# Kernel optimization log

Hardware: AMD Instinct MI355X
Metric: run time of the kernel (lower is better)

## Reference

```python
import jax, jax.numpy as jnp
import numpy as np

S, B, D, H, WIN, L = 8192, 4, 512, 8, 64, 6
HD = D // H
EPS = 1e-5


def setup_inputs() -> dict:
    key = jax.random.key(0)
    ks = jax.random.split(key, 6)
    s = 0.02
    return {
        "src": jax.random.normal(ks[0], (S, B, D), jnp.float32),
        "Wqkv": jax.random.normal(ks[1], (L, 3 * D, D), jnp.float32) * s,
        "bqkv": jnp.zeros((L, 3 * D), jnp.float32),
        "Wo": jax.random.normal(ks[2], (L, D, D), jnp.float32) * s,
        "bo": jnp.zeros((L, D), jnp.float32),
        "W1": jax.random.normal(ks[3], (L, 4 * D, D), jnp.float32) * s,
        "bf1": jnp.zeros((L, 4 * D), jnp.float32),
        "W2": jax.random.normal(ks[4], (L, D, 4 * D), jnp.float32) * s,
        "bf2": jnp.zeros((L, D), jnp.float32),
        "g1": jnp.ones((L, D), jnp.float32),
        "beta1": jnp.zeros((L, D), jnp.float32),
        "g2": jnp.ones((L, D), jnp.float32),
        "beta2": jnp.zeros((L, D), jnp.float32),
    }


def layernorm(x, g, b):
    m = jnp.mean(x, axis=-1, keepdims=True)
    v = jnp.mean(jnp.square(x - m), axis=-1, keepdims=True)
    return (x - m) * jax.lax.rsqrt(v + EPS) * g + b


def _forward(src, Wqkv, bqkv, Wo, bo, W1, bf1, W2, bf2, g1, beta1, g2, beta2):
    NW = S // WIN
    scale = 1.0 / np.sqrt(HD)
    x = src
    for l in range(L):
        qkv = x @ Wqkv[l].T + bqkv[l]                      # (S,B,3D)
        q, k, v = jnp.split(qkv, 3, axis=-1)
        win = lambda t: t.reshape(NW, WIN, B, H, HD)       # (NW,W,B,H,hd)
        q = win(q) * scale
        k = win(k)
        v = win(v)
        att = jax.nn.softmax(jnp.einsum('nqbhd,nkbhd->nbhqk', q, k), axis=-1)
        o = jnp.einsum('nbhqk,nkbhd->nqbhd', att, v).reshape(S, B, D)
        o = o @ Wo[l].T + bo[l]
        x = layernorm(x + o, g1[l], beta1[l])
        # FFN with ReLU (hidden = 4*d_model)
        f = jax.nn.relu(x @ W1[l].T + bf1[l]) @ W2[l].T + bf2[l]
        x = layernorm(x + f, g2[l], beta2[l])
    return x


def reference(src, Wqkv, bqkv, Wo, bo, W1, bf1, W2, bf2, g1, beta1, g2, beta2):
    return _forward(src, Wqkv, bqkv, Wo, bo, W1, bf1, W2, bf2, g1, beta1, g2, beta2)
```

## Files before the change

### kernel.cpp

```cpp
#include <hip/hip_runtime.h>
#include <hip/hip_bf16.h>

typedef __bf16 bf16x8 __attribute__((ext_vector_type(8)));
typedef float f32x4 __attribute__((ext_vector_type(4)));

static constexpr int NT = 32768;
static constexpr int D_ = 512;
static constexpr int D3 = 1536;
static constexpr int DF = 2048;
static constexpr int L_ = 6;

#define AS1 __attribute__((address_space(1)))
#define AS3 __attribute__((address_space(3)))

__device__ __forceinline__ void gload_lds16(const void* g, void* l) {
  __builtin_amdgcn_global_load_lds((const AS1 void*)g, (AS3 void*)l, 16, 0, 0);
}

template<int K, int NTN, bool RELU>
__global__ __launch_bounds__(256, 3) void gemm128g(
    const __hip_bfloat16* __restrict__ A,
    const __hip_bfloat16* __restrict__ Wp,
    const float* __restrict__ bias,
    __hip_bfloat16* __restrict__ Cout) {
  __shared__ __align__(16) char lds[32768];
  const int t = threadIdx.x;
  const int l = t & 63, w = t >> 6;
  const int lrow = l & 15, lhi = l >> 4;
  const int wr = w >> 1, wc = w & 1;

  const int lin = blockIdx.x;
  const int wg = (lin & 7) * ((int)gridDim.x >> 3) + (lin >> 3);
  const int tm0 = (wg / NTN) * 128, tn0 = (wg % NTN) * 128;

  constexpr int NKT = K / 64;
  constexpr int NIT = NKT / 2;
  constexpr int N = NTN * 128;

  const int srow = t >> 3;
  const int sun = t & 7;
  const int u8 = (sun ^ (srow & 7)) << 3;
  const __hip_bfloat16* sA = A + (size_t)(tm0 + srow) * K + u8;
  const __hip_bfloat16* sA2 = sA + (size_t)64 * K;

  const char* bpB = (const char*)(Wp + (size_t)((tn0 >> 6) + wc) * NKT * 4096) +
                    l * 16;

  const int lo = lrow * 128;
  const int x0 = (lhi ^ (lrow & 7)) << 4;
  const int x1 = ((4 + lhi) ^ (lrow & 7)) << 4;
  const char* pA[2][2];
  pA[0][0] = lds + wr * 8192 + lo + x0;
  pA[0][1] = lds + wr * 8192 + lo + x1;
  pA[1][0] = lds + 16384 + wr * 8192 + lo + x0;
  pA[1][1] = lds + 16384 + wr * 8192 + lo + x1;

  auto stageA = [&](int p, const __hip_bfloat16* s0, const __hip_bfloat16* s1) {
    char* d0 = lds + p * 16384 + w * 1024;
    gload_lds16(s0, d0);
    gload_lds16(s0 + (size_t)32 * K, d0 + 4096);
    char* d1 = lds + p * 16384 + 8192 + w * 1024;
    gload_lds16(s1, d1);
    gload_lds16(s1 + (size_t)32 * K, d1 + 4096);
  };
  auto loadB = [&](bf16x8 (&bf)[4][2], const char* q) {
    const char* q2 = q + 4096;
#pragma unroll
    for (int n = 0; n < 2; ++n)
#pragma unroll
      for (int ks = 0; ks < 2; ++ks) {
        bf[n][ks] = *(const bf16x8*)(q + (n * 2 + ks) * 1024);
        bf[2 + n][ks] = *(const bf16x8*)(q2 + (n * 2 + ks) * 1024);
      }
  };

  f32x4 acc[4][4] = {};
  bf16x8 bfA[4][2], bfB[4][2], af[2][2];

  stageA(0, sA, sA2);
  __builtin_amdgcn_sched_barrier(0);
  loadB(bfA, bpB);
  asm volatile("s_waitcnt vmcnt(8)" ::: "memory");
  __builtin_amdgcn_sched_barrier(0);
  __builtin_amdgcn_s_barrier();

#define SUB(P, BF, MB)                                                      \
  {                                                                          \
    _Pragma("unroll") for (int ks = 0; ks < 2; ++ks) {                       \
      af[0][ks] = *(const bf16x8*)(pA[P][ks] + (MB) * 2048);                 \
      af[1][ks] = *(const bf16x8*)(pA[P][ks] + (MB + 1) * 2048);             \
    }                                                                        \
    _Pragma("unroll") for (int n = 0; n < 4; ++n)                            \
        _Pragma("unroll") for (int ks = 0; ks < 2; ++ks) {                   \
      acc[MB][n] = __builtin_amdgcn_mfma_f32_16x16x32_bf16(                  \
          af[0][ks], BF[n][ks], acc[MB][n], 0, 0, 0);                        \
      acc[MB + 1][n] = __builtin_amdgcn_mfma_f32_16x16x32_bf16(              \
          af[1][ks], BF[n][ks], acc[MB + 1][n], 0, 0, 0);                    \
    }                                                                        \
  }
#define CLOSE(VM)                                                           \
  if (VM) asm volatile("s_waitcnt vmcnt(8)" ::: "memory");                  \
  else asm volatile("s_waitcnt vmcnt(0)" ::: "memory");                     \
  asm volatile("s_waitcnt lgkmcnt(0)" ::: "memory");                        \
  __builtin_amdgcn_sched_barrier(0);                                        \
  __builtin_amdgcn_s_barrier();

  const __hip_bfloat16* sAe = sA;
  const __hip_bfloat16* sA2e = sA2;
  const char* qbe = bpB;
  for (int it = 0; it < NIT; ++it) {
    const bool more = (it + 1 < NIT);
    stageA(1, sAe + 64, sA2e + 64);
    __builtin_amdgcn_sched_barrier(0);
    loadB(bfB, qbe + 8192);
    SUB(0, bfA, 0)
    SUB(0, bfA, 2)
    CLOSE(1)
    if (more) {
      stageA(0, sAe + 128, sA2e + 128);
      __builtin_amdgcn_sched_barrier(0);
      loadB(bfA, qbe + 16384);
    }
    SUB(1, bfB, 0)
    SUB(1, bfB, 2)
    CLOSE(more)
    sAe += 128;
    sA2e += 128;
    qbe += 16384;
  }
#undef SUB
#undef CLOSE

  char* ep = lds + w * 8192;
#pragma unroll
  for (int n = 0; n < 4; ++n) {
    float bv = bias[tn0 + wc * 64 + n * 16 + lrow];
#pragma unroll
    for (int m = 0; m < 4; ++m)
#pragma unroll
      for (int j = 0; j < 4; ++j) {
        float v = acc[m][n][j] + bv;
        if (RELU) v = fmaxf(v, 0.f);
        int row = m * 16 + lhi * 4 + j;
        int col = n * 16 + lrow;
        *(__hip_bfloat16*)(ep + row * 128 + (((col >> 3) ^ (row & 7)) << 4) +
                           (col & 7) * 2) = __float2bfloat16(v);
      }
  }
  __builtin_amdgcn_sched_barrier(0);
  const int er = l >> 3, ec = l & 7;
#pragma unroll
  for (int q = 0; q < 8; ++q) {
    int r = q * 8 + er;
    uint4 vv = *(const uint4*)(ep + r * 128 + ((ec ^ (r & 7)) << 4));
    *(uint4*)&Cout[(size_t)(tm0 + wr * 64 + r) * N + tn0 + wc * 64 + ec * 8] = vv;
  }
}

__global__ __launch_bounds__(128) void attn_win(
    const __hip_bfloat16* __restrict__ qkv, __hip_bfloat16* __restrict__ o) {
  __shared__ __align__(16) char lds[2 * 18432];
  const int t = threadIdx.x, l = t & 63, w = t >> 6;
  char* vt = lds + w * 18432;
  char* pl = vt + 9216;
  const int wid = blockIdx.x * 2 + w;
  const int h = wid & 7, b = (wid >> 3) & 3, nw = wid >> 5;
  const int lrow = l & 15, lhi = l >> 4;
  const __hip_bfloat16* qp = qkv + (size_t)(nw * 256 + b) * 1536 + h * 64;
  const __hip_bfloat16* kp = qp + 512;
  const __hip_bfloat16* vp = qp + 1024;

  {
    const int d0 = (l & 7) * 8;
    const int r0 = l >> 3;
#pragma unroll
    for (int i = 0; i < 8; ++i) {
      int r = r0 + i * 8;
      union { uint4 u; __hip_bfloat16 e[8]; } vv;
      vv.u = *(const uint4*)(vp + (size_t)r * 6144 + d0);
#pragma unroll
      for (int j = 0; j < 8; ++j)
        *(__hip_bfloat16*)(vt + ((d0 + j) * 72 + r) * 2) = vv.e[j];
    }
  }

  bf16x8 qf[4][2], kf[4][2];
#pragma unroll
  for (int mi = 0; mi < 4; ++mi)
#pragma unroll
    for (int ks = 0; ks < 2; ++ks) {
      int r = mi * 16 + lrow;
      int d = ks * 32 + lhi * 8;
      qf[mi][ks] = __builtin_bit_cast(bf16x8, *(const uint4*)(qp + (size_t)r * 6144 + d));
      kf[mi][ks] = __builtin_bit_cast(bf16x8, *(const uint4*)(kp + (size_t)r * 6144 + d));
    }

  f32x4 s[4][4] = {};
#pragma unroll
  for (int mi = 0; mi < 4; ++mi)
#pragma unroll
    for (int ni = 0; ni < 4; ++ni) {
      s[mi][ni] = __builtin_amdgcn_mfma_f32_16x16x32_bf16(qf[mi][0], kf[ni][0], s[mi][ni], 0, 0, 0);
      s[mi][ni] = __builtin_amdgcn_mfma_f32_16x16x32_bf16(qf[mi][1], kf[ni][1], s[mi][ni], 0, 0, 0);
    }

#pragma unroll
  for (int mi = 0; mi < 4; ++mi)
#pragma unroll
    for (int j = 0; j < 4; ++j) {
      float mx = s[mi][0][j];
#pragma unroll
      for (int ni = 1; ni < 4; ++ni) mx = fmaxf(mx, s[mi][ni][j]);
      mx = fmaxf(mx, __shfl_xor(mx, 1));
      mx = fmaxf(mx, __shfl_xor(mx, 2));
      mx = fmaxf(mx, __shfl_xor(mx, 4));
      mx = fmaxf(mx, __shfl_xor(mx, 8));
      float p[4], sum = 0.f;
#pragma unroll
      for (int ni = 0; ni < 4; ++ni) { p[ni] = __expf(s[mi][ni][j] - mx); sum += p[ni]; }
      sum += __shfl_xor(sum, 1);
      sum += __shfl_xor(sum, 2);
      sum += __shfl_xor(sum, 4);
      sum += __shfl_xor(sum, 8);
      float inv = 1.f / sum;
      int row = mi * 16 + lhi * 4 + j;
#pragma unroll
      for (int ni = 0; ni < 4; ++ni)
        *(__hip_bfloat16*)(pl + (row * 72 + ni * 16 + lrow) * 2) =
            __float2bfloat16(p[ni] * inv);
    }

  bf16x8 pf[4][2], vf[4][2];
#pragma unroll
  for (int mi = 0; mi < 4; ++mi)
#pragma unroll
    for (int ks = 0; ks < 2; ++ks)
      pf[mi][ks] = *(const bf16x8*)(pl + ((mi * 16 + lrow) * 72 + ks * 32 + lhi * 8) * 2);
#pragma unroll
  for (int ni = 0; ni < 4; ++ni)
#pragma unroll
    for (int ks = 0; ks < 2; ++ks)
      vf[ni][ks] = *(const bf16x8*)(vt + ((ni * 16 + lrow) * 72 + ks * 32 + lhi * 8) * 2);

  f32x4 acc[4][4] = {};
#pragma unroll
  for (int mi = 0; mi < 4; ++mi)
#pragma unroll
    for (int ni = 0; ni < 4; ++ni) {
      acc[mi][ni] = __builtin_amdgcn_mfma_f32_16x16x32_bf16(pf[mi][0], vf[ni][0], acc[mi][ni], 0, 0, 0);
      acc[mi][ni] = __builtin_amdgcn_mfma_f32_16x16x32_bf16(pf[mi][1], vf[ni][1], acc[mi][ni], 0, 0, 0);
    }

  __hip_bfloat16* op = o + (size_t)(nw * 256 + b) * 512 + h * 64;
#pragma unroll
  for (int mi = 0; mi < 4; ++mi)
#pragma unroll
    for (int ni = 0; ni < 4; ++ni) {
      int col = ni * 16 + lrow;
#pragma unroll
      for (int j = 0; j < 4; ++j) {
        int row = mi * 16 + lhi * 4 + j;
        op[(size_t)row * 2048 + col] = __float2bfloat16(acc[mi][ni][j]);
      }
    }
}

template<bool LAST>
__global__ __launch_bounds__(256) void ln_res_b(
    __hip_bfloat16* __restrict__ xb, const __hip_bfloat16* __restrict__ f,
    const float* __restrict__ g, const float* __restrict__ be,
    float* __restrict__ xout) {
  const int w = threadIdx.x >> 6, l = threadIdx.x & 63;
  const size_t row = (size_t)blockIdx.x * 4 + w;
  const int c = l * 8;
  union { uint4 u; __hip_bfloat16 e[8]; } xa, fa;
  xa.u = *(const uint4*)(xb + row * 512 + c);
  fa.u = *(const uint4*)(f + row * 512 + c);
  float v[8];
#pragma unroll
  for (int j = 0; j < 8; ++j)
    v[j] = __bfloat162float(xa.e[j]) + __bfloat162float(fa.e[j]);
  float sum = 0.f, sq = 0.f;
#pragma unroll
  for (int j = 0; j < 8; ++j) { sum += v[j]; sq += v[j] * v[j]; }
#pragma unroll
  for (int m = 1; m < 64; m <<= 1) {
    sum += __shfl_xor(sum, m);
    sq += __shfl_xor(sq, m);
  }
  float mean = sum * (1.f / 512.f);
  float var = sq * (1.f / 512.f) - mean * mean;
  float rs = rsqrtf(var + 1e-5f);
  float4 g0 = *(const float4*)(g + c);
  float4 g1v = *(const float4*)(g + c + 4);
  float4 e0 = *(const float4*)(be + c);
  float4 e1 = *(const float4*)(be + c + 4);
  float gg[8] = {g0.x, g0.y, g0.z, g0.w, g1v.x, g1v.y, g1v.z, g1v.w};
  float ee[8] = {e0.x, e0.y, e0.z, e0.w, e1.x, e1.y, e1.z, e1.w};
  float y[8];
  union { uint4 u; __hip_bfloat16 e[8]; } hb;
#pragma unroll
  for (int j = 0; j < 8; ++j) {
    y[j] = (v[j] - mean) * rs * gg[j] + ee[j];
    hb.e[j] = __float2bfloat16(y[j]);
  }
  *(uint4*)(xb + row * 512 + c) = hb.u;
  if (LAST) {
    float4 o0 = {y[0], y[1], y[2], y[3]};
    float4 o1 = {y[4], y[5], y[6], y[7]};
    *(float4*)(xout + row * 512 + c) = o0;
    *(float4*)(xout + row * 512 + c + 4) = o1;
  }
}

__global__ void convw(const float* __restrict__ s, __hip_bfloat16* __restrict__ o) {
  int i = blockIdx.x * 256 + threadIdx.x;
  float4 v = ((const float4*)s)[i];
  __hip_bfloat16 hb[4] = {__float2bfloat16(v.x), __float2bfloat16(v.y),
                          __float2bfloat16(v.z), __float2bfloat16(v.w)};
  ((uint2*)o)[i] = *(uint2*)hb;
}

template<int K, int Nw, bool SCALEQ>
__global__ void convs(const float* __restrict__ s, __hip_bfloat16* __restrict__ o) {
  int i = blockIdx.x * 256 + threadIdx.x;
  int e = i * 4;
  int layer = e / (Nw * K);
  int rem = e - layer * (Nw * K);
  int r = rem / K, c = rem - r * K;
  float4 v = ((const float4*)s)[i];
  float sc = (SCALEQ && r < 512) ? 0.125f : 1.f;
  int didx = layer * (Nw * K) + ((r >> 6) * (K >> 6) + (c >> 6)) * 4096 +
             (((r >> 4) & 3) * 2 + ((c >> 5) & 1)) * 512 + ((c >> 3) & 3) * 128 +
             (r & 15) * 8 + (c & 7);
  __hip_bfloat16 hb[4] = {__float2bfloat16(v.x * sc), __float2bfloat16(v.y * sc),
                          __float2bfloat16(v.z * sc), __float2bfloat16(v.w * sc)};
  *(uint2*)(o + didx) = *(uint2*)hb;
}

__global__ void scaleb(const float* __restrict__ b, float* __restrict__ o) {
  int i = blockIdx.x * 256 + threadIdx.x;
  o[i] = b[i] * (((i % 1536) < 512) ? 0.125f : 1.f);
}

extern "C" void kernel_launch(void* const* d_in, const int* in_sizes, int n_in,
                              void* d_out, int out_size, void* d_ws, size_t ws_size,
                              hipStream_t stream) {
  const float* src  = (const float*)d_in[0];
  const float* Wqkv = (const float*)d_in[1];
  const float* bqkv = (const float*)d_in[2];
  const float* Wo   = (const float*)d_in[3];
  const float* bo   = (const float*)d_in[4];
  const float* W1   = (const float*)d_in[5];
  const float* bf1  = (const float*)d_in[6];
  const float* W2   = (const float*)d_in[7];
  const float* bf2  = (const float*)d_in[8];
  const float* g1   = (const float*)d_in[9];
  const float* be1  = (const float*)d_in[10];
  const float* g2   = (const float*)d_in[11];
  const float* be2  = (const float*)d_in[12];
  float* xout = (float*)d_out;

  char* ws = (char*)d_ws;
  size_t off = 0;
  auto alloc = [&](size_t bytes) {
    char* p = ws + off;
    off += (bytes + 255) & ~(size_t)255;
    return p;
  };

  const size_t wq_b = (size_t)L_ * D3 * D_ * 2;
  const size_t wo_b = (size_t)L_ * D_ * D_ * 2;
  const size_t w1_b = (size_t)L_ * DF * D_ * 2;
  const size_t w2_b = (size_t)L_ * D_ * DF * 2;
  const size_t xb_b = (size_t)NT * 512 * 2;
  auto al = [](size_t v) { return (v + 255) & ~(size_t)255; };
  const size_t persist =
      al(wq_b) + al(wo_b) + al(w1_b) + al(w2_b) + al(L_ * D3 * 4) + al(xb_b);

  int CT = NT;
  while (CT > 2048 && persist + (size_t)CT * 5120 + 65536 > ws_size) CT >>= 1;

  __hip_bfloat16* wqkvb = (__hip_bfloat16*)alloc(wq_b);
  __hip_bfloat16* wob   = (__hip_bfloat16*)alloc(wo_b);
  __hip_bfloat16* w1b   = (__hip_bfloat16*)alloc(w1_b);
  __hip_bfloat16* w2b   = (__hip_bfloat16*)alloc(w2_b);
  float*          bqs   = (float*)alloc((size_t)L_ * D3 * 4);
  __hip_bfloat16* xb    = (__hip_bfloat16*)alloc(xb_b);
  __hip_bfloat16* R     = (__hip_bfloat16*)alloc((size_t)CT * 2048 * 2);
  __hip_bfloat16* OB    = (__hip_bfloat16*)alloc((size_t)CT * 512 * 2);

  convw<<<NT * 512 / 4 / 256, 256, 0, stream>>>(src, xb);
  convs<512, 1536, true><<<L_ * D3 * D_ / 4 / 256, 256, 0, stream>>>(Wqkv, wqkvb);
  convs<512, 512, false><<<L_ * D_ * D_ / 4 / 256, 256, 0, stream>>>(Wo, wob);
  convs<512, 2048, false><<<L_ * DF * D_ / 4 / 256, 256, 0, stream>>>(W1, w1b);
  convs<2048, 512, false><<<L_ * D_ * DF / 4 / 256, 256, 0, stream>>>(W2, w2b);
  scaleb<<<L_ * D3 / 256, 256, 0, stream>>>(bqkv, bqs);

  const int nch = NT / CT;
  for (int c = 0; c < nch; ++c) {
    __hip_bfloat16* xm = xb + (size_t)c * CT * 512;
    float* xo = xout + (size_t)c * CT * 512;
    for (int l = 0; l < L_; ++l) {
      gemm128g<512, 12, false><<<(CT / 128) * 12, 256, 0, stream>>>(
          xm, wqkvb + (size_t)l * D3 * D_, bqs + l * D3, R);
      attn_win<<<CT / 16, 128, 0, stream>>>(R, OB);
      gemm128g<512, 4, false><<<(CT / 128) * 4, 256, 0, stream>>>(
          OB, wob + (size_t)l * D_ * D_, bo + l * D_, R);
      ln_res_b<false><<<CT / 4, 256, 0, stream>>>(xm, R, g1 + l * D_,
                                                  be1 + l * D_, xo);
      gemm128g<512, 16, true><<<(CT / 128) * 16, 256, 0, stream>>>(
          xm, w1b + (size_t)l * DF * D_, bf1 + l * DF, R);
      gemm128g<2048, 4, false><<<(CT / 128) * 4, 256, 0, stream>>>(
          R, w2b + (size_t)l * D_ * DF, bf2 + l * D_, OB);
      if (l == L_ - 1)
        ln_res_b<true><<<CT / 4, 256, 0, stream>>>(xm, OB, g2 + l * D_,
                                                   be2 + l * D_, xo);
      else
        ln_res_b<false><<<CT / 4, 256, 0, stream>>>(xm, OB, g2 + l * D_,
                                                    be2 + l * D_, xo);
    }
  }
}
```

Measured before the change: 1.812 ms.

## Deepen GEMM A-tile staging to four LDS buffers with two-tile prefetch

Grows the GEMM's A-operand LDS ring from two to four 16KB buffers. The main loop becomes four phases per iteration, and A tiles are prefetched two k-steps ahead instead of one. The explicit vmcnt waits inside the loop are dropped and only lgkmcnt waits plus barriers remain, so ordering now depends on the compiler's waits for the B register loads. The aim is to hide more global latency, at the cost of 64KB LDS per block and lowering the launch-bounds occupancy hint from 3 to 2.

```diff
diff --git a/kernel.cpp b/kernel.cpp
--- a/kernel.cpp
+++ b/kernel.cpp
@@ -18,12 +18,12 @@
 }
 
 template<int K, int NTN, bool RELU>
-__global__ __launch_bounds__(256, 3) void gemm128g(
+__global__ __launch_bounds__(256, 2) void gemm128g(
     const __hip_bfloat16* __restrict__ A,
     const __hip_bfloat16* __restrict__ Wp,
     const float* __restrict__ bias,
     __hip_bfloat16* __restrict__ Cout) {
-  __shared__ __align__(16) char lds[32768];
+  __shared__ __align__(16) char lds[65536];
   const int t = threadIdx.x;
   const int l = t & 63, w = t >> 6;
   const int lrow = l & 15, lhi = l >> 4;
@@ -34,7 +34,7 @@
   const int tm0 = (wg / NTN) * 128, tn0 = (wg % NTN) * 128;
 
   constexpr int NKT = K / 64;
-  constexpr int NIT = NKT / 2;
+  constexpr int NI4 = NKT / 4;
   constexpr int N = NTN * 128;
 
   const int srow = t >> 3;
@@ -49,11 +49,12 @@
   const int lo = lrow * 128;
   const int x0 = (lhi ^ (lrow & 7)) << 4;
   const int x1 = ((4 + lhi) ^ (lrow & 7)) << 4;
-  const char* pA[2][2];
-  pA[0][0] = lds + wr * 8192 + lo + x0;
-  pA[0][1] = lds + wr * 8192 + lo + x1;
-  pA[1][0] = lds + 16384 + wr * 8192 + lo + x0;
-  pA[1][1] = lds + 16384 + wr * 8192 + lo + x1;
+  const char* pA[4][2];
+#pragma unroll
+  for (int p = 0; p < 4; ++p) {
+    pA[p][0] = lds + p * 16384 + wr * 8192 + lo + x0;
+    pA[p][1] = lds + p * 16384 + wr * 8192 + lo + x1;
+  }
 
   auto stageA = [&](int p, const __hip_bfloat16* s0, const __hip_bfloat16* s1) {
     char* d0 = lds + p * 16384 + w * 1024;
@@ -78,9 +79,10 @@
   bf16x8 bfA[4][2], bfB[4][2], af[2][2];
 
   stageA(0, sA, sA2);
+  stageA(1, sA + 64, sA2 + 64);
   __builtin_amdgcn_sched_barrier(0);
   loadB(bfA, bpB);
-  asm volatile("s_waitcnt vmcnt(8)" ::: "memory");
+  asm volatile("s_waitcnt vmcnt(0)" ::: "memory");
   __builtin_amdgcn_sched_barrier(0);
   __builtin_amdgcn_s_barrier();
 
@@ -98,38 +100,33 @@
           af[1][ks], BF[n][ks], acc[MB + 1][n], 0, 0, 0);                    \
     }                                                                        \
   }
-#define CLOSE(VM)                                                           \
-  if (VM) asm volatile("s_waitcnt vmcnt(8)" ::: "memory");                  \
-  else asm volatile("s_waitcnt vmcnt(0)" ::: "memory");                     \
-  asm volatile("s_waitcnt lgkmcnt(0)" ::: "memory");                        \
-  __builtin_amdgcn_sched_barrier(0);                                        \
-  __builtin_amdgcn_s_barrier();
+#define PHASE(J, SBUF, DOST, ST, LBDST, DOLB, BT, BCONS)                    \
+  {                                                                          \
+    if (DOST) stageA(SBUF, sAe + (ST) * 64, sA2e + (ST) * 64);               \
+    __builtin_amdgcn_sched_barrier(0);                                       \
+    if (DOLB) loadB(LBDST, qbe + (size_t)(BT) * 8192);                       \
+    SUB(J, BCONS, 0)                                                         \
+    SUB(J, BCONS, 2)                                                         \
+    asm volatile("s_waitcnt lgkmcnt(0)" ::: "memory");                       \
+    __builtin_amdgcn_sched_barrier(0);                                       \
+    __builtin_amdgcn_s_barrier();                                            \
+  }
 
   const __hip_bfloat16* sAe = sA;
   const __hip_bfloat16* sA2e = sA2;
   const char* qbe = bpB;
-  for (int it = 0; it < NIT; ++it) {
-    const bool more = (it + 1 < NIT);
-    stageA(1, sAe + 64, sA2e + 64);
-    __builtin_amdgcn_sched_barrier(0);
-    loadB(bfB, qbe + 8192);
-    SUB(0, bfA, 0)
-    SUB(0, bfA, 2)
-    CLOSE(1)
-    if (more) {
-      stageA(0, sAe + 128, sA2e + 128);
-      __builtin_amdgcn_sched_barrier(0);
-      loadB(bfA, qbe + 16384);
-    }
-    SUB(1, bfB, 0)
-    SUB(1, bfB, 2)
-    CLOSE(more)
-    sAe += 128;
-    sA2e += 128;
-    qbe += 16384;
-  }
+  for (int it = 0; it < NI4; ++it) {
+    const bool more = (it + 1 < NI4);
+    PHASE(0, 2, true, 2, bfB, true, 1, bfA)
+    PHASE(1, 3, true, 3, bfA, true, 2, bfB)
+    PHASE(2, 0, more, 4, bfB, true, 3, bfA)
+    PHASE(3, 1, more, 5, bfA, more, 4, bfB)
+    sAe += 256;
+    sA2e += 256;
+    qbe += 32768;
+  }
+#undef PHASE
 #undef SUB
-#undef CLOSE
 
   char* ep = lds + w * 8192;
 #pragma unroll
```

Result: slower. 1.938 ms (+6.9%).
